# Performance work log

Hardware: AMD Instinct MI355X
Metric: run time of the kernel (lower is better)

Reference implementation:

```python
import jax, jax.numpy as jnp
import numpy as np

D_MODEL = 1024
NUM_HEADS = 16
D_FF = 4096
EPS = 1e-5


def setup_inputs() -> dict:
    key = jax.random.key(0)
    ks = jax.random.split(key, 8)
    B, S, D = 4, 2048, D_MODEL
    s = 1.0 / np.sqrt(D)
    return {
        "x": jax.random.normal(ks[0], (B, S, D), jnp.float32),
        "ln1_w": jnp.ones((D,), jnp.float32),
        "ln2_w": jnp.ones((D,), jnp.float32),
        "wq": jax.random.normal(ks[1], (D, D), jnp.float32) * s,
        "wk": jax.random.normal(ks[2], (D, D), jnp.float32) * s,
        "wv": jax.random.normal(ks[3], (D, D), jnp.float32) * s,
        "wo": jax.random.normal(ks[4], (D, D), jnp.float32) * s,
        "w1": jax.random.normal(ks[5], (D_FF, D), jnp.float32) * s,
        "w2": jax.random.normal(ks[6], (D, D_FF), jnp.float32) * (1.0 / np.sqrt(D_FF)),
    }


def rmsnorm(a, w):
    # (a * w) / sqrt(mean(a^2) + eps)  -- matches torch module exactly
    denom = jnp.sqrt(jnp.mean(jnp.square(a), axis=-1, keepdims=True) + EPS)
    return a * w / denom


def attention(x, wq, wk, wv, wo):
    B, S, D = x.shape
    H, dk = NUM_HEADS, D // NUM_HEADS
    q = (x @ wq.T).reshape(B, S, H, dk).transpose(0, 2, 1, 3)  # B H S dk
    k = (x @ wk.T).reshape(B, S, H, dk).transpose(0, 2, 1, 3)
    v = (x @ wv.T).reshape(B, S, H, dk).transpose(0, 2, 1, 3)
    scores = jnp.einsum("bhqd,bhkd->bhqk", q, k) / np.sqrt(dk)
    causal = jnp.triu(jnp.ones((S, S), bool), k=1)
    scores = jnp.where(causal, -jnp.inf, scores)
    probs = jax.nn.softmax(scores, axis=-1)
    out = jnp.einsum("bhqk,bhkd->bhqd", probs, v)
    out = out.transpose(0, 2, 1, 3).reshape(B, S, D)
    return out @ wo.T


def ffn(x, w1, w2):
    h = x @ w1.T
    h = 0.5 * h * (1.0 + jax.lax.erf(h / np.sqrt(2.0).astype(np.float32)))
    return h @ w2.T


def reference(x, ln1_w, ln2_w, wq, wk, wv, wo, w1, w2):
    y = x + attention(rmsnorm(x, ln1_w), wq, wk, wv, wo)
    return y + ffn(rmsnorm(y, ln2_w), w1, w2)
```

## Files before the change

kernel.cpp:

```cpp
#include <hip/hip_runtime.h>

#define DM    1024
#define DFF   4096
#define SEQ   2048
#define BATCH 4
#define NROWS (BATCH * SEQ)
#define HEADS 16
#define DKH   64
#define KSTR  (2 * DM)

typedef __attribute__((ext_vector_type(4))) float          f32x4;
typedef __attribute__((ext_vector_type(8))) __bf16         bf16x8;
typedef __attribute__((ext_vector_type(8))) unsigned short u16x8;
typedef __attribute__((ext_vector_type(4))) unsigned short u16x4;

static __device__ __forceinline__ unsigned short f2bf(float f) {
  unsigned u = __builtin_bit_cast(unsigned, f);
  u += 0x7fffu + ((u >> 16) & 1u);
  return (unsigned short)(u >> 16);
}

struct CvtJobs {
  const float* src[6];
  unsigned short* dst[6];
};
__constant__ const unsigned c_cum[6] = {262144u, 524288u, 786432u, 1048576u, 2097152u, 3145728u};
#define CVT_BLOCKS 12288u

__global__ __launch_bounds__(256) void k_pre(CvtJobs jobs,
                                             const float* __restrict__ x,
                                             const float* __restrict__ ln1,
                                             unsigned short* __restrict__ xn) {
  if (blockIdx.x < CVT_BLOCKS) {
    const unsigned i = blockIdx.x * 256u + threadIdx.x;
    int j = 0;
#pragma unroll
    for (int s = 0; s < 6; ++s) j += (i >= c_cum[s]) ? 1 : 0;
    const unsigned base = (j == 0) ? 0u : c_cum[j - 1];
    const unsigned loc  = i - base;
    float4 v = reinterpret_cast<const float4*>(jobs.src[j])[loc];
    ushort4 o;
    o.x = f2bf(v.x); o.y = f2bf(v.y); o.z = f2bf(v.z); o.w = f2bf(v.w);
    reinterpret_cast<ushort4*>(jobs.dst[j])[loc] = o;
  } else {
    const int row = (int)(blockIdx.x - CVT_BLOCKS);
    const float4 v = reinterpret_cast<const float4*>(x + (size_t)row * DM)[threadIdx.x];
    float ss = v.x * v.x + v.y * v.y + v.z * v.z + v.w * v.w;
#pragma unroll
    for (int off = 32; off > 0; off >>= 1) ss += __shfl_down(ss, off);
    __shared__ float red[4];
    if ((threadIdx.x & 63) == 0) red[threadIdx.x >> 6] = ss;
    __syncthreads();
    const float tot  = red[0] + red[1] + red[2] + red[3];
    const float rden = rsqrtf(tot * (1.0f / DM) + 1e-5f);
    const float4 wv = reinterpret_cast<const float4*>(ln1)[threadIdx.x];
    ushort4 o;
    o.x = f2bf(v.x * wv.x * rden);
    o.y = f2bf(v.y * wv.y * rden);
    o.z = f2bf(v.z * wv.z * rden);
    o.w = f2bf(v.w * wv.w * rden);
    reinterpret_cast<ushort4*>(xn + (size_t)row * DM)[threadIdx.x] = o;
  }
}

__global__ __launch_bounds__(256) void k_rmsnorm(const float* __restrict__ x,
                                                 const float* __restrict__ w,
                                                 unsigned short* __restrict__ out) {
  const int row = blockIdx.x;
  const float4 v = reinterpret_cast<const float4*>(x + (size_t)row * DM)[threadIdx.x];
  float ss = v.x * v.x + v.y * v.y + v.z * v.z + v.w * v.w;
#pragma unroll
  for (int off = 32; off > 0; off >>= 1) ss += __shfl_down(ss, off);
  __shared__ float red[4];
  if ((threadIdx.x & 63) == 0) red[threadIdx.x >> 6] = ss;
  __syncthreads();
  const float tot  = red[0] + red[1] + red[2] + red[3];
  const float rden = rsqrtf(tot * (1.0f / DM) + 1e-5f);
  const float4 wv = reinterpret_cast<const float4*>(w)[threadIdx.x];
  ushort4 o;
  o.x = f2bf(v.x * wv.x * rden);
  o.y = f2bf(v.y * wv.y * rden);
  o.z = f2bf(v.z * wv.z * rden);
  o.w = f2bf(v.w * wv.w * rden);
  reinterpret_cast<ushort4*>(out + (size_t)row * DM)[threadIdx.x] = o;
}

__device__ __forceinline__ void gemm_body_128_64(const unsigned short* __restrict__ A,
                                                 const unsigned short* __restrict__ B,
                                                 unsigned short* __restrict__ C,
                                                 int M, int N, int K, bool prescale,
                                                 unsigned vbid, unsigned vgx, unsigned vgy,
                                                 unsigned short* AsP, unsigned short* BsP) {
  const int t  = threadIdx.x;
  const int w  = t >> 6;
  const int l  = t & 63;
  const int wr = w >> 1, wc = w & 1;
  const int lr = l & 15, lk = l >> 4;

  const unsigned cpx = (vgx * vgy) >> 3;
  const unsigned sw  = (vbid & 7) * cpx + (vbid >> 3);
  const int m0 = (int)(sw / vgx) * 128;
  const int n0 = (int)(sw % vgx) * 128;

  const int srow8 = l >> 3;
  const int g     = l & 7;

  auto stage = [&](int buf, int k0) {
#pragma unroll
    for (int i = 0; i < 4; ++i) {
      const int row = i * 32 + w * 8 + srow8;
      const int sg  = g ^ (row & 7);
      const unsigned short* ga = A + (size_t)(m0 + row) * K + k0 + 8 * sg;
      __builtin_amdgcn_global_load_lds((__attribute__((address_space(1))) void*)ga,
                                       (__attribute__((address_space(3))) void*)(AsP + buf * 8192 + i * 2048 + w * 512),
                                       16, 0, 0);
      const unsigned short* gb = B + (size_t)(n0 + row) * K + k0 + 8 * sg;
      __builtin_amdgcn_global_load_lds((__attribute__((address_space(1))) void*)gb,
                                       (__attribute__((address_space(3))) void*)(BsP + buf * 8192 + i * 2048 + w * 512),
                                       16, 0, 0);
    }
  };

  f32x4 acc[4][4] = {};

  stage(0, 0);
  const int nIt = K >> 6;
  for (int it = 0; it < nIt; ++it) {
    const int buf = it & 1;
    __syncthreads();
    if (it + 1 < nIt) stage(buf ^ 1, (it + 1) << 6);

#pragma unroll
    for (int kk = 0; kk < 2; ++kk) {
      bf16x8 af[4], bf[4];
#pragma unroll
      for (int m = 0; m < 4; ++m)
        af[m] = *reinterpret_cast<const bf16x8*>(
            AsP + buf * 8192 + (wr * 64 + m * 16 + lr) * 64 + 8 * ((4 * kk + lk) ^ (lr & 7)));
#pragma unroll
      for (int n = 0; n < 4; ++n)
        bf[n] = *reinterpret_cast<const bf16x8*>(
            BsP + buf * 8192 + (wc * 64 + n * 16 + lr) * 64 + 8 * ((4 * kk + lk) ^ (lr & 7)));
#pragma unroll
      for (int m = 0; m < 4; ++m)
#pragma unroll
        for (int n = 0; n < 4; ++n)
          acc[m][n] = __builtin_amdgcn_mfma_f32_16x16x32_bf16(af[m], bf[n], acc[m][n], 0, 0, 0);
    }
  }

#pragma unroll
  for (int m = 0; m < 4; ++m) {
#pragma unroll
    for (int n = 0; n < 4; ++n) {
#pragma unroll
      for (int r = 0; r < 4; ++r) {
        const size_t row = (size_t)(m0 + wr * 64 + m * 16 + lk * 4 + r);
        const size_t col = (size_t)(n0 + wc * 64 + n * 16 + lr);
        const float sc = (prescale && col < DM) ? 0.18033688011f : 1.0f;
        C[row * N + col] = f2bf(acc[m][n][r] * sc);
      }
    }
  }
}

__global__ __launch_bounds__(256, 2) void k_qkvt(const unsigned short* __restrict__ xn,
                                                 const unsigned short* __restrict__ wqkb,
                                                 unsigned short* __restrict__ qk,
                                                 const unsigned short* __restrict__ wvb,
                                                 unsigned short* __restrict__ vtb) {
  alignas(16) __shared__ unsigned short As[2][128 * 64];
  alignas(16) __shared__ unsigned short Bs[2][128 * 64];
  const unsigned bid = blockIdx.x;
  if (bid < 1024u) {
    gemm_body_128_64(xn, wqkb, qk, NROWS, 2 * DM, DM, true, bid, 16, 64, &As[0][0], &Bs[0][0]);
  } else {
    gemm_body_128_64(wvb, xn, vtb, DM, NROWS, DM, false, bid - 1024u, 64, 8, &As[0][0], &Bs[0][0]);
  }
}

template <int EPI, int TN, int BK>
__global__ __launch_bounds__(256, 2) void k_gemm_nt(const unsigned short* __restrict__ A,
                                                    const unsigned short* __restrict__ B,
                                                    void* __restrict__ Cv,
                                                    const float* __restrict__ res,
                                                    int M, int N, int K) {
  constexpr int NW = TN / 128;
  alignas(16) __shared__ unsigned short As[2][128 * BK];
  alignas(16) __shared__ unsigned short Bs[2][128 * NW * BK];
  const int t  = threadIdx.x;
  const int w  = t >> 6;
  const int l  = t & 63;
  const int wr = w >> 1, wc = w & 1;
  const int lr = l & 15, lk = l >> 4;

  const unsigned bid = blockIdx.y * gridDim.x + blockIdx.x;
  const unsigned cpx = (gridDim.x * gridDim.y) >> 3;
  const unsigned sw  = (bid & 7) * cpx + (bid >> 3);
  const int m0 = (int)(sw / gridDim.x) * 128;
  const int n0 = (int)(sw % gridDim.x) * TN;

  auto stage = [&](int buf, int k0) {
    if constexpr (BK == 32) {
      const int srow = t >> 2;
      const int sgr  = (t & 3) ^ (srow & 3);
#pragma unroll
      for (int r = 0; r < 2; ++r) {
        const unsigned short* ga = A + (size_t)(m0 + r * 64 + srow) * K + k0 + 8 * sgr;
        __builtin_amdgcn_global_load_lds((__attribute__((address_space(1))) void*)ga,
                                         (__attribute__((address_space(3))) void*)(&As[buf][r * 2048 + w * 512]),
                                         16, 0, 0);
      }
#pragma unroll
      for (int r = 0; r < 2 * NW; ++r) {
        const unsigned short* gb = B + (size_t)(n0 + r * 64 + srow) * K + k0 + 8 * sgr;
        __builtin_amdgcn_global_load_lds((__attribute__((address_space(1))) void*)gb,
                                         (__attribute__((address_space(3))) void*)(&Bs[buf][r * 2048 + w * 512]),
                                         16, 0, 0);
      }
    } else {
      const int srow8 = l >> 3;
      const int g     = l & 7;
#pragma unroll
      for (int i = 0; i < 4; ++i) {
        const int row = i * 32 + w * 8 + srow8;
        const int sg  = g ^ (row & 7);
        const unsigned short* ga = A + (size_t)(m0 + row) * K + k0 + 8 * sg;
        __builtin_amdgcn_global_load_lds((__attribute__((address_space(1))) void*)ga,
                                         (__attribute__((address_space(3))) void*)(&As[buf][i * 2048 + w * 512]),
                                         16, 0, 0);
        const unsigned short* gb = B + (size_t)(n0 + row) * K + k0 + 8 * sg;
        __builtin_amdgcn_global_load_lds((__attribute__((address_space(1))) void*)gb,
                                         (__attribute__((address_space(3))) void*)(&Bs[buf][i * 2048 + w * 512]),
                                         16, 0, 0);
      }
    }
  };

  f32x4 acc[4][4 * NW] = {};

  stage(0, 0);
  const int nIt = K / BK;
  for (int it = 0; it < nIt; ++it) {
    const int buf = it & 1;
    __syncthreads();
    if (it + 1 < nIt) stage(buf ^ 1, (it + 1) * BK);

    if constexpr (BK == 32) {
      bf16x8 af[4], bf[4 * NW];
#pragma unroll
      for (int m = 0; m < 4; ++m)
        af[m] = *reinterpret_cast<const bf16x8*>(
            &As[buf][(wr * 64 + m * 16 + lr) * 32 + 8 * (lk ^ (lr & 3))]);
#pragma unroll
      for (int n = 0; n < 4 * NW; ++n)
        bf[n] = *reinterpret_cast<const bf16x8*>(
            &Bs[buf][(wc * 64 * NW + n * 16 + lr) * 32 + 8 * (lk ^ (lr & 3))]);
#pragma unroll
      for (int m = 0; m < 4; ++m)
#pragma unroll
        for (int n = 0; n < 4 * NW; ++n)
          acc[m][n] = __builtin_amdgcn_mfma_f32_16x16x32_bf16(af[m], bf[n], acc[m][n], 0, 0, 0);
    } else {
#pragma unroll
      for (int kk = 0; kk < 2; ++kk) {
        bf16x8 af[4], bf[4];
#pragma unroll
        for (int m = 0; m < 4; ++m)
          af[m] = *reinterpret_cast<const bf16x8*>(
              &As[buf][(wr * 64 + m * 16 + lr) * 64 + 8 * ((4 * kk + lk) ^ (lr & 7))]);
#pragma unroll
        for (int n = 0; n < 4; ++n)
          bf[n] = *reinterpret_cast<const bf16x8*>(
              &Bs[buf][(wc * 64 + n * 16 + lr) * 64 + 8 * ((4 * kk + lk) ^ (lr & 7))]);
#pragma unroll
        for (int m = 0; m < 4; ++m)
#pragma unroll
          for (int n = 0; n < 4; ++n)
            acc[m][n] = __builtin_amdgcn_mfma_f32_16x16x32_bf16(af[m], bf[n], acc[m][n], 0, 0, 0);
      }
    }
  }

#pragma unroll
  for (int m = 0; m < 4; ++m) {
#pragma unroll
    for (int n = 0; n < 4 * NW; ++n) {
#pragma unroll
      for (int r = 0; r < 4; ++r) {
        const size_t row = (size_t)(m0 + wr * 64 + m * 16 + lk * 4 + r);
        const size_t col = (size_t)(n0 + wc * 64 * NW + n * 16 + lr);
        const float a = acc[m][n][r];
        if constexpr (EPI == 1) {
          ((float*)Cv)[row * N + col] = a + res[row * N + col];
        } else {
          const float h2 = a * a;
          const float e  = exp2f(a * (2.30221535f + 0.10295355f * h2));
          const float g  = a - a / (e + 1.0f);
          ((unsigned short*)Cv)[row * N + col] = f2bf(g);
        }
      }
    }
  }
}

__global__ __launch_bounds__(256, 3) void k_attn(const unsigned short* __restrict__ QK,
                                                 const unsigned short* __restrict__ VT,
                                                 unsigned short* __restrict__ O) {
  const int h   = blockIdx.x;
  const int qtA = blockIdx.y;
  const int qtB = 31 - qtA;
  const int b   = blockIdx.z;
  const int t  = threadIdx.x, w = t >> 6, l = t & 63;
  const int lr = l & 15, lk = l >> 4;
  const size_t rowB = (size_t)b * SEQ;
  const int hoff  = h * DKH;
  const int qw2[2] = { qtA * 64 + 16 * w, qtB * 64 + 16 * w };

  alignas(16) __shared__ unsigned short Ks[128 * 64];
  alignas(16) __shared__ unsigned short Vt[64 * 128];
  alignas(16) __shared__ unsigned short Ps[2][4][16 * 64];

  char* const KsB = (char*)Ks;
  char* const VtB = (char*)Vt;

  auto stage = [&](int kb2) {
#pragma unroll
    for (int i = 0; i < 4; ++i) {
      const int krow = 32 * w + 8 * i + (l >> 3);
      const int sgk  = (l & 7) ^ (krow & 7);
      const unsigned short* gk = QK + (size_t)(rowB + kb2 + krow) * KSTR + DM + hoff + 8 * sgk;
      __builtin_amdgcn_global_load_lds((__attribute__((address_space(1))) void*)gk,
                                       (__attribute__((address_space(3))) void*)(KsB + w * 4096 + i * 1024),
                                       16, 0, 0);
      const int vrow = 16 * w + 4 * i + (l >> 4);
      const int sgv  = (l & 15) ^ (vrow & 15);
      const unsigned short* gv = VT + (size_t)(hoff + vrow) * NROWS + rowB + kb2 + 8 * sgv;
      __builtin_amdgcn_global_load_lds((__attribute__((address_space(1))) void*)gv,
                                       (__attribute__((address_space(3))) void*)(VtB + w * 4096 + i * 1024),
                                       16, 0, 0);
    }
  };

  bf16x8 qf[2][2];
#pragma unroll
  for (int s = 0; s < 2; ++s)
#pragma unroll
    for (int kk = 0; kk < 2; ++kk)
      qf[s][kk] = *reinterpret_cast<const bf16x8*>(
          QK + (rowB + qw2[s] + lr) * KSTR + hoff + 32 * kk + 8 * lk);

  f32x4 oacc[2][4] = {};
  float mrun[2] = {-1e30f, -1e30f};
  float lrun[2] = {0.0f, 0.0f};

  const int ktmax = qtB >> 1;
  for (int kt = 0; kt <= ktmax; ++kt) {
    const int kbase = kt * 128;
    __syncthreads();
    stage(kbase);
    __syncthreads();

#pragma unroll
    for (int h2 = 0; h2 < 2; ++h2) {
      const int kb = kbase + 64 * h2;
      const bool act[2] = { kb <= qw2[0] + 15, kb <= qw2[1] + 15 };
      if (!act[0] && !act[1]) continue;
      const char* Kc = KsB + h2 * 8192;

      f32x4 sacc[2][4] = {};
      __builtin_amdgcn_s_setprio(1);
#pragma unroll
      for (int tt = 0; tt < 4; ++tt) {
        bf16x8 kf0 = *reinterpret_cast<const bf16x8*>(Kc + (16 * tt + lr) * 128 + 16 * ((lk + 0) ^ (lr & 7)));
        bf16x8 kf1 = *reinterpret_cast<const bf16x8*>(Kc + (16 * tt + lr) * 128 + 16 * ((lk + 4) ^ (lr & 7)));
#pragma unroll
        for (int s = 0; s < 2; ++s) {
          if (!act[s]) continue;
          sacc[s][tt] = __builtin_amdgcn_mfma_f32_16x16x32_bf16(kf0, qf[s][0], sacc[s][tt], 0, 0, 0);
          sacc[s][tt] = __builtin_amdgcn_mfma_f32_16x16x32_bf16(kf1, qf[s][1], sacc[s][tt], 0, 0, 0);
        }
      }
      __builtin_amdgcn_s_setprio(0);

#pragma unroll
      for (int s = 0; s < 2; ++s) {
        if (!act[s]) continue;
        const int qw = qw2[s];
        char* const PsSB = (char*)(Ps[s][w]);
        const int qg = qw + lr;
        float sv[4][4];
        if (kb + 63 > qw) {
#pragma unroll
          for (int tt = 0; tt < 4; ++tt)
#pragma unroll
            for (int r = 0; r < 4; ++r) {
              const int kg = kb + 16 * tt + 4 * lk + r;
              sv[tt][r] = (kg > qg) ? -1e30f : sacc[s][tt][r];
            }
        } else {
#pragma unroll
          for (int tt = 0; tt < 4; ++tt)
#pragma unroll
            for (int r = 0; r < 4; ++r) sv[tt][r] = sacc[s][tt][r];
        }
        const float a0 = fmaxf(fmaxf(sv[0][0], sv[0][1]), sv[0][2]);
        const float a1 = fmaxf(fmaxf(sv[0][3], sv[1][0]), sv[1][1]);
        const float a2 = fmaxf(fmaxf(sv[1][2], sv[1][3]), sv[2][0]);
        const float a3 = fmaxf(fmaxf(sv[2][1], sv[2][2]), sv[2][3]);
        const float a4 = fmaxf(fmaxf(sv[3][0], sv[3][1]), sv[3][2]);
        float tm = fmaxf(fmaxf(fmaxf(a0, a1), a2), fmaxf(fmaxf(a3, a4), sv[3][3]));
        tm = fmaxf(tm, __shfl_xor(tm, 16));
        tm = fmaxf(tm, __shfl_xor(tm, 32));
        float mref = mrun[s];
        if (__any(tm > mref + 8.0f)) {
          const float mnew  = fmaxf(mref, tm);
          const float alpha = exp2f(mref - mnew);
#pragma unroll
          for (int r = 0; r < 4; ++r) {
            const float ar = __shfl(alpha, 4 * lk + r);
#pragma unroll
            for (int dn = 0; dn < 4; ++dn) oacc[s][dn][r] *= ar;
          }
          lrun[s] *= alpha;
          mrun[s] = mnew;
          mref = mnew;
        }
        float p[4][4];
        unsigned short pb[4][4];
#pragma unroll
        for (int tt = 0; tt < 4; ++tt)
#pragma unroll
          for (int r = 0; r < 4; ++r) {
            p[tt][r] = exp2f(sv[tt][r] - mref);
            pb[tt][r] = __builtin_bit_cast(unsigned short, static_cast<__bf16>(p[tt][r]));
          }
        float t0 = (p[0][0] + p[0][1]) + (p[0][2] + p[0][3]);
        float t1 = (p[1][0] + p[1][1]) + (p[1][2] + p[1][3]);
        float t2 = (p[2][0] + p[2][1]) + (p[2][2] + p[2][3]);
        float t3 = (p[3][0] + p[3][1]) + (p[3][2] + p[3][3]);
        float ts = (t0 + t1) + (t2 + t3);
        ts += __shfl_xor(ts, 16);
        ts += __shfl_xor(ts, 32);
        lrun[s] += ts;
#pragma unroll
        for (int tt = 0; tt < 4; ++tt) {
          u16x4 pw = {pb[tt][0], pb[tt][1], pb[tt][2], pb[tt][3]};
          *reinterpret_cast<u16x4*>(
              PsSB + lr * 128 + ((32 * tt + 8 * lk) ^ (16 * (lr & 7)))) = pw;
        }
      }

      asm volatile("" ::: "memory");

#pragma unroll
      for (int kk = 0; kk < 2; ++kk) {
        bf16x8 vf[4];
#pragma unroll
        for (int dn = 0; dn < 4; ++dn)
          vf[dn] = *reinterpret_cast<const bf16x8*>(
              VtB + (16 * dn + lr) * 256 + 16 * ((8 * h2 + 4 * kk + lk) ^ lr));
        __builtin_amdgcn_s_setprio(1);
#pragma unroll
        for (int s = 0; s < 2; ++s) {
          if (!act[s]) continue;
          char* const PsSB = (char*)(Ps[s][w]);
          bf16x8 pa = *reinterpret_cast<const bf16x8*>(
              PsSB + lr * 128 + ((64 * kk + 16 * lk) ^ (16 * (lr & 7))));
#pragma unroll
          for (int dn = 0; dn < 4; ++dn)
            oacc[s][dn] = __builtin_amdgcn_mfma_f32_16x16x32_bf16(pa, vf[dn], oacc[s][dn], 0, 0, 0);
        }
        __builtin_amdgcn_s_setprio(0);
      }

      asm volatile("" ::: "memory");
    }
  }

#pragma unroll
  for (int s = 0; s < 2; ++s)
#pragma unroll
    for (int r = 0; r < 4; ++r) {
      const float li = 1.0f / __shfl(lrun[s], 4 * lk + r);
      const size_t row = rowB + qw2[s] + 4 * lk + r;
#pragma unroll
      for (int dn = 0; dn < 4; ++dn)
        O[row * DM + hoff + 16 * dn + lr] = f2bf(oacc[s][dn][r] * li);
    }
}

extern "C" void kernel_launch(void* const* d_in, const int* in_sizes, int n_in,
                              void* d_out, int out_size, void* d_ws, size_t ws_size,
                              hipStream_t stream) {
  const float* x   = (const float*)d_in[0];
  const float* ln1 = (const float*)d_in[1];
  const float* ln2 = (const float*)d_in[2];
  const float* wq  = (const float*)d_in[3];
  const float* wk  = (const float*)d_in[4];
  const float* wv  = (const float*)d_in[5];
  const float* wo  = (const float*)d_in[6];
  const float* w1  = (const float*)d_in[7];
  const float* w2  = (const float*)d_in[8];

  char* ws = (char*)d_ws;
  size_t off = 0;
  auto take = [&](size_t bytes) { void* p = ws + off; off += bytes; return p; };
  unsigned short* wqkb = (unsigned short*)take((size_t)2 * DM * DM * 2);
  unsigned short* wvb  = (unsigned short*)take((size_t)DM * DM * 2);
  unsigned short* wob  = (unsigned short*)take((size_t)DM * DM * 2);
  unsigned short* w1b  = (unsigned short*)take((size_t)DFF * DM * 2);
  unsigned short* w2b  = (unsigned short*)take((size_t)DM * DFF * 2);
  unsigned short* qk   = (unsigned short*)take((size_t)NROWS * 2 * DM * 2);
  unsigned short* xn   = (unsigned short*)take((size_t)NROWS * DM * 2);
  unsigned short* vtb  = (unsigned short*)take((size_t)DM * NROWS * 2);
  float*          yb   = (float*)take((size_t)NROWS * DM * 4);
  unsigned short* hb   = (unsigned short*)take((size_t)NROWS * DFF * 2);
  unsigned short* yn   = qk;

  CvtJobs jobs;
  jobs.src[0] = wq;  jobs.dst[0] = wqkb;
  jobs.src[1] = wk;  jobs.dst[1] = wqkb + (size_t)DM * DM;
  jobs.src[2] = wv;  jobs.dst[2] = wvb;
  jobs.src[3] = wo;  jobs.dst[3] = wob;
  jobs.src[4] = w1;  jobs.dst[4] = w1b;
  jobs.src[5] = w2;  jobs.dst[5] = w2b;

  k_pre<<<dim3(CVT_BLOCKS + NROWS), dim3(256), 0, stream>>>(jobs, x, ln1, xn);

  k_qkvt<<<dim3(1536), dim3(256), 0, stream>>>(xn, wqkb, qk, wvb, vtb);

  k_attn<<<dim3(HEADS, 16, BATCH), dim3(256), 0, stream>>>(qk, vtb, xn);

  k_gemm_nt<1, 128, 64><<<dim3(DM / 128, NROWS / 128), dim3(256), 0, stream>>>(
      xn, wob, yb, x, NROWS, DM, DM);

  k_rmsnorm<<<dim3(NROWS), dim3(256), 0, stream>>>(yb, ln2, yn);

  k_gemm_nt<2, 256, 32><<<dim3(DFF / 256, NROWS / 128), dim3(256), 0, stream>>>(
      yn, w1b, hb, nullptr, NROWS, DFF, DM);
  k_gemm_nt<1, 128, 64><<<dim3(DM / 128, NROWS / 128), dim3(256), 0, stream>>>(
      hb, w2b, (float*)d_out, yb, NROWS, DM, DFF);
}
```

Before: 373.3 us.

## Defer wo/w1/w2 conversion into attention launch and retile QKV GEMM to BK32

The prologue kernel now converts only wq/wk/wv to bf16. The wo/w1/w2 conversions move into extra tail blocks of the attention kernel, so that memory-bound work can overlap with compute-heavy attention blocks. The QKV GEMM body is rewritten with a K-step of 32 and templated N tile width: 256 for the QK projection, giving fewer blocks, and 128 for V^T. This halves LDS per stage but doubles the barrier count per K. Attention blocks are flattened into a 1D grid index, and the conversion blocks risk sharing CUs with attention blocks.

```diff
diff --git a/kernel.cpp b/kernel.cpp
--- a/kernel.cpp
+++ b/kernel.cpp
@@ -20,30 +20,28 @@
   return (unsigned short)(u >> 16);
 }
 
-struct CvtJobs {
-  const float* src[6];
-  unsigned short* dst[6];
-};
-__constant__ const unsigned c_cum[6] = {262144u, 524288u, 786432u, 1048576u, 2097152u, 3145728u};
-#define CVT_BLOCKS 12288u
-
-__global__ __launch_bounds__(256) void k_pre(CvtJobs jobs,
+#define CVT1_BLOCKS 3072u
+
+__global__ __launch_bounds__(256) void k_pre(const float* __restrict__ wq,
+                                             const float* __restrict__ wk,
+                                             const float* __restrict__ wv,
+                                             unsigned short* __restrict__ wqkb,
+                                             unsigned short* __restrict__ wvb,
                                              const float* __restrict__ x,
                                              const float* __restrict__ ln1,
                                              unsigned short* __restrict__ xn) {
-  if (blockIdx.x < CVT_BLOCKS) {
+  if (blockIdx.x < CVT1_BLOCKS) {
     const unsigned i = blockIdx.x * 256u + threadIdx.x;
-    int j = 0;
-#pragma unroll
-    for (int s = 0; s < 6; ++s) j += (i >= c_cum[s]) ? 1 : 0;
-    const unsigned base = (j == 0) ? 0u : c_cum[j - 1];
-    const unsigned loc  = i - base;
-    float4 v = reinterpret_cast<const float4*>(jobs.src[j])[loc];
+    const float* src; unsigned short* dst; unsigned loc;
+    if (i < 262144u)      { src = wq; dst = wqkb;            loc = i; }
+    else if (i < 524288u) { src = wk; dst = wqkb + 1048576u; loc = i - 262144u; }
+    else                  { src = wv; dst = wvb;             loc = i - 524288u; }
+    float4 v = reinterpret_cast<const float4*>(src)[loc];
     ushort4 o;
     o.x = f2bf(v.x); o.y = f2bf(v.y); o.z = f2bf(v.z); o.w = f2bf(v.w);
-    reinterpret_cast<ushort4*>(jobs.dst[j])[loc] = o;
+    reinterpret_cast<ushort4*>(dst)[loc] = o;
   } else {
-    const int row = (int)(blockIdx.x - CVT_BLOCKS);
+    const int row = (int)(blockIdx.x - CVT1_BLOCKS);
     const float4 v = reinterpret_cast<const float4*>(x + (size_t)row * DM)[threadIdx.x];
     float ss = v.x * v.x + v.y * v.y + v.z * v.z + v.w * v.w;
 #pragma unroll
@@ -53,12 +51,12 @@
     __syncthreads();
     const float tot  = red[0] + red[1] + red[2] + red[3];
     const float rden = rsqrtf(tot * (1.0f / DM) + 1e-5f);
-    const float4 wv = reinterpret_cast<const float4*>(ln1)[threadIdx.x];
+    const float4 wv4 = reinterpret_cast<const float4*>(ln1)[threadIdx.x];
     ushort4 o;
-    o.x = f2bf(v.x * wv.x * rden);
-    o.y = f2bf(v.y * wv.y * rden);
-    o.z = f2bf(v.z * wv.z * rden);
-    o.w = f2bf(v.w * wv.w * rden);
+    o.x = f2bf(v.x * wv4.x * rden);
+    o.y = f2bf(v.y * wv4.y * rden);
+    o.z = f2bf(v.z * wv4.z * rden);
+    o.w = f2bf(v.w * wv4.w * rden);
     reinterpret_cast<ushort4*>(xn + (size_t)row * DM)[threadIdx.x] = o;
   }
 }
@@ -85,79 +83,79 @@
   reinterpret_cast<ushort4*>(out + (size_t)row * DM)[threadIdx.x] = o;
 }
 
-__device__ __forceinline__ void gemm_body_128_64(const unsigned short* __restrict__ A,
-                                                 const unsigned short* __restrict__ B,
-                                                 unsigned short* __restrict__ C,
-                                                 int M, int N, int K, bool prescale,
-                                                 unsigned vbid, unsigned vgx, unsigned vgy,
-                                                 unsigned short* AsP, unsigned short* BsP) {
+template <int TN, bool PRESCALE>
+__device__ __forceinline__ void gemm_body_bk32(const unsigned short* __restrict__ A,
+                                               const unsigned short* __restrict__ B,
+                                               unsigned short* __restrict__ C,
+                                               int M, int N, int K,
+                                               unsigned vbid, unsigned vgx, unsigned vnb,
+                                               unsigned short* AsP, unsigned short* BsP) {
+  constexpr int NW = TN / 128;
   const int t  = threadIdx.x;
   const int w  = t >> 6;
   const int l  = t & 63;
   const int wr = w >> 1, wc = w & 1;
   const int lr = l & 15, lk = l >> 4;
 
-  const unsigned cpx = (vgx * vgy) >> 3;
+  const unsigned cpx = vnb >> 3;
   const unsigned sw  = (vbid & 7) * cpx + (vbid >> 3);
   const int m0 = (int)(sw / vgx) * 128;
-  const int n0 = (int)(sw % vgx) * 128;
-
-  const int srow8 = l >> 3;
-  const int g     = l & 7;
+  const int n0 = (int)(sw % vgx) * TN;
+
+  const int srow = t >> 2;
+  const int sgr  = (t & 3) ^ (srow & 3);
 
   auto stage = [&](int buf, int k0) {
 #pragma unroll
-    for (int i = 0; i < 4; ++i) {
-      const int row = i * 32 + w * 8 + srow8;
-      const int sg  = g ^ (row & 7);
-      const unsigned short* ga = A + (size_t)(m0 + row) * K + k0 + 8 * sg;
+    for (int r = 0; r < 2; ++r) {
+      const unsigned short* ga = A + (size_t)(m0 + r * 64 + srow) * K + k0 + 8 * sgr;
       __builtin_amdgcn_global_load_lds((__attribute__((address_space(1))) void*)ga,
-                                       (__attribute__((address_space(3))) void*)(AsP + buf * 8192 + i * 2048 + w * 512),
+                                       (__attribute__((address_space(3))) void*)(AsP + buf * 4096 + r * 2048 + w * 512),
                                        16, 0, 0);
-      const unsigned short* gb = B + (size_t)(n0 + row) * K + k0 + 8 * sg;
+    }
+#pragma unroll
+    for (int r = 0; r < 2 * NW; ++r) {
+      const unsigned short* gb = B + (size_t)(n0 + r * 64 + srow) * K + k0 + 8 * sgr;
       __builtin_amdgcn_global_load_lds((__attribute__((address_space(1))) void*)gb,
-                                       (__attribute__((address_space(3))) void*)(BsP + buf * 8192 + i * 2048 + w * 512),
+                                       (__attribute__((address_space(3))) void*)(BsP + buf * 4096 * NW + r * 2048 + w * 512),
                                        16, 0, 0);
     }
   };
 
-  f32x4 acc[4][4] = {};
+  f32x4 acc[4][4 * NW] = {};
 
   stage(0, 0);
-  const int nIt = K >> 6;
+  const int nIt = K >> 5;
   for (int it = 0; it < nIt; ++it) {
     const int buf = it & 1;
     __syncthreads();
-    if (it + 1 < nIt) stage(buf ^ 1, (it + 1) << 6);
-
-#pragma unroll
-    for (int kk = 0; kk < 2; ++kk) {
-      bf16x8 af[4], bf[4];
-#pragma unroll
-      for (int m = 0; m < 4; ++m)
-        af[m] = *reinterpret_cast<const bf16x8*>(
-            AsP + buf * 8192 + (wr * 64 + m * 16 + lr) * 64 + 8 * ((4 * kk + lk) ^ (lr & 7)));
-#pragma unroll
-      for (int n = 0; n < 4; ++n)
-        bf[n] = *reinterpret_cast<const bf16x8*>(
-            BsP + buf * 8192 + (wc * 64 + n * 16 + lr) * 64 + 8 * ((4 * kk + lk) ^ (lr & 7)));
-#pragma unroll
-      for (int m = 0; m < 4; ++m)
-#pragma unroll
-        for (int n = 0; n < 4; ++n)
-          acc[m][n] = __builtin_amdgcn_mfma_f32_16x16x32_bf16(af[m], bf[n], acc[m][n], 0, 0, 0);
-    }
+    if (it + 1 < nIt) stage(buf ^ 1, (it + 1) << 5);
+
+    bf16x8 af[4], bf[4 * NW];
+#pragma unroll
+    for (int m = 0; m < 4; ++m)
+      af[m] = *reinterpret_cast<const bf16x8*>(
+          AsP + buf * 4096 + (wr * 64 + m * 16 + lr) * 32 + 8 * (lk ^ (lr & 3)));
+#pragma unroll
+    for (int n = 0; n < 4 * NW; ++n)
+      bf[n] = *reinterpret_cast<const bf16x8*>(
+          BsP + buf * 4096 * NW + (wc * 64 * NW + n * 16 + lr) * 32 + 8 * (lk ^ (lr & 3)));
+#pragma unroll
+    for (int m = 0; m < 4; ++m)
+#pragma unroll
+      for (int n = 0; n < 4 * NW; ++n)
+        acc[m][n] = __builtin_amdgcn_mfma_f32_16x16x32_bf16(af[m], bf[n], acc[m][n], 0, 0, 0);
   }
 
 #pragma unroll
   for (int m = 0; m < 4; ++m) {
 #pragma unroll
-    for (int n = 0; n < 4; ++n) {
+    for (int n = 0; n < 4 * NW; ++n) {
 #pragma unroll
       for (int r = 0; r < 4; ++r) {
         const size_t row = (size_t)(m0 + wr * 64 + m * 16 + lk * 4 + r);
-        const size_t col = (size_t)(n0 + wc * 64 + n * 16 + lr);
-        const float sc = (prescale && col < DM) ? 0.18033688011f : 1.0f;
+        const size_t col = (size_t)(n0 + wc * 64 * NW + n * 16 + lr);
+        const float sc = (PRESCALE && col < DM) ? 0.18033688011f : 1.0f;
         C[row * N + col] = f2bf(acc[m][n][r] * sc);
       }
     }
@@ -169,13 +167,13 @@
                                                  unsigned short* __restrict__ qk,
                                                  const unsigned short* __restrict__ wvb,
                                                  unsigned short* __restrict__ vtb) {
-  alignas(16) __shared__ unsigned short As[2][128 * 64];
-  alignas(16) __shared__ unsigned short Bs[2][128 * 64];
+  alignas(16) __shared__ unsigned short As[2][128 * 32];
+  alignas(16) __shared__ unsigned short Bs[2][256 * 32];
   const unsigned bid = blockIdx.x;
-  if (bid < 1024u) {
-    gemm_body_128_64(xn, wqkb, qk, NROWS, 2 * DM, DM, true, bid, 16, 64, &As[0][0], &Bs[0][0]);
+  if (bid < 512u) {
+    gemm_body_bk32<256, true >(xn, wqkb, qk, NROWS, 2 * DM, DM, bid, 8, 512, &As[0][0], &Bs[0][0]);
   } else {
-    gemm_body_128_64(wvb, xn, vtb, DM, NROWS, DM, false, bid - 1024u, 64, 8, &As[0][0], &Bs[0][0]);
+    gemm_body_bk32<128, false>(wvb, xn, vtb, DM, NROWS, DM, bid - 512u, 64, 512, &As[0][0], &Bs[0][0]);
   }
 }
 
@@ -304,13 +302,35 @@
   }
 }
 
+#define ATTN_BLOCKS 1024u
+#define CVT2_BLOCKS 9216u
+
 __global__ __launch_bounds__(256, 3) void k_attn(const unsigned short* __restrict__ QK,
                                                  const unsigned short* __restrict__ VT,
-                                                 unsigned short* __restrict__ O) {
-  const int h   = blockIdx.x;
-  const int qtA = blockIdx.y;
+                                                 unsigned short* __restrict__ O,
+                                                 const float* __restrict__ wo,
+                                                 const float* __restrict__ w1,
+                                                 const float* __restrict__ w2,
+                                                 unsigned short* __restrict__ wob,
+                                                 unsigned short* __restrict__ w1b,
+                                                 unsigned short* __restrict__ w2b) {
+  if (blockIdx.x >= ATTN_BLOCKS) {
+    const unsigned i = (blockIdx.x - ATTN_BLOCKS) * 256u + threadIdx.x;
+    const float* src; unsigned short* dst; unsigned loc;
+    if (i < 262144u)       { src = wo; dst = wob; loc = i; }
+    else if (i < 1310720u) { src = w1; dst = w1b; loc = i - 262144u; }
+    else                   { src = w2; dst = w2b; loc = i - 1310720u; }
+    float4 v = reinterpret_cast<const float4*>(src)[loc];
+    ushort4 o;
+    o.x = f2bf(v.x); o.y = f2bf(v.y); o.z = f2bf(v.z); o.w = f2bf(v.w);
+    reinterpret_cast<ushort4*>(dst)[loc] = o;
+    return;
+  }
+
+  const int h   = blockIdx.x & 15;
+  const int qtA = (blockIdx.x >> 4) & 15;
   const int qtB = 31 - qtA;
-  const int b   = blockIdx.z;
+  const int b   = blockIdx.x >> 8;
   const int t  = threadIdx.x, w = t >> 6, l = t & 63;
   const int lr = l & 15, lk = l >> 4;
   const size_t rowB = (size_t)b * SEQ;
@@ -518,19 +538,12 @@
   unsigned short* hb   = (unsigned short*)take((size_t)NROWS * DFF * 2);
   unsigned short* yn   = qk;
 
-  CvtJobs jobs;
-  jobs.src[0] = wq;  jobs.dst[0] = wqkb;
-  jobs.src[1] = wk;  jobs.dst[1] = wqkb + (size_t)DM * DM;
-  jobs.src[2] = wv;  jobs.dst[2] = wvb;
-  jobs.src[3] = wo;  jobs.dst[3] = wob;
-  jobs.src[4] = w1;  jobs.dst[4] = w1b;
-  jobs.src[5] = w2;  jobs.dst[5] = w2b;
-
-  k_pre<<<dim3(CVT_BLOCKS + NROWS), dim3(256), 0, stream>>>(jobs, x, ln1, xn);
-
-  k_qkvt<<<dim3(1536), dim3(256), 0, stream>>>(xn, wqkb, qk, wvb, vtb);
-
-  k_attn<<<dim3(HEADS, 16, BATCH), dim3(256), 0, stream>>>(qk, vtb, xn);
+  k_pre<<<dim3(CVT1_BLOCKS + NROWS), dim3(256), 0, stream>>>(wq, wk, wv, wqkb, wvb, x, ln1, xn);
+
+  k_qkvt<<<dim3(1024), dim3(256), 0, stream>>>(xn, wqkb, qk, wvb, vtb);
+
+  k_attn<<<dim3(ATTN_BLOCKS + CVT2_BLOCKS), dim3(256), 0, stream>>>(
+      qk, vtb, xn, wo, w1, w2, wob, w1b, w2b);
 
   k_gemm_nt<1, 128, 64><<<dim3(DM / 128, NROWS / 128), dim3(256), 0, stream>>>(
       xn, wob, yb, x, NROWS, DM, DM);
```

After: 369.6 us. No clear change (-1.0%).
